# Performance work log

Measured on AMD Instinct MI355X. Metric: run time of the kernel, lower is better.

The kernel has to match this reference:

```python
import jax, jax.numpy as jnp
import numpy as np

B, D, H1, H2 = 512, 1024, 512, 128

def setup_inputs() -> dict:
    key = jax.random.key(0)
    ks = jax.random.split(key, 3)
    x = jax.random.normal(ks[0], (B, D), dtype=jnp.float32)
    W1 = jax.random.normal(ks[1], (H1, D), dtype=jnp.float32)
    W2 = jax.random.normal(ks[2], (H2, H1), dtype=jnp.float32)
    b1 = jnp.full((H1,), 0.1, dtype=jnp.float32)
    b2 = jnp.full((H2,), 0.1, dtype=jnp.float32)
    b3 = jnp.full((H1,), 0.1, dtype=jnp.float32)
    b_r = jnp.full((D,), 0.1, dtype=jnp.float32)
    return {"x": x, "W1": W1, "b1": b1, "W2": W2, "b2": b2, "b3": b3, "b_r": b_r}

def reference(x, W1, b1, W2, b2, b3, b_r):
    # encoder
    c1 = jax.nn.sigmoid(x @ W1.T + b1)          # [B, H1]
    c2 = jax.nn.sigmoid(c1 @ W2.T + b2)         # [B, H2]
    # decoder (tied weights)
    c3 = jax.nn.sigmoid(c2 @ W2 + b3)           # [B, H1]
    recover = c3 @ W1 + b_r                     # [B, D]
    # Jacobian of code w.r.t. x, batched (replaces per-sample diag+matmul loop):
    # Jac[b] = diag(c2'(b)) @ W2 @ diag(c1'(b)) @ W1
    s1p = c1 * (1.0 - c1)                       # [B, H1]
    s2p = c2 * (1.0 - c2)                       # [B, H2]
    M = s2p[:, :, None] * W2[None, :, :] * s1p[:, None, :]   # [B, H2, H1]
    Jac = jnp.einsum('bhk,kd->bhd', M, W1)      # [B, H2, D]
    return (recover, c2, Jac)
```

## Files before the change

kernel.cpp:

```cpp
#include <hip/hip_runtime.h>


typedef _Float16 f16x8 __attribute__((ext_vector_type(8)));
typedef _Float16 f16x4 __attribute__((ext_vector_type(4)));
typedef float    f32x4 __attribute__((ext_vector_type(4)));
typedef float    f32x2 __attribute__((ext_vector_type(2)));

__device__ __forceinline__ void gld_lds16(const _Float16* src, _Float16* dst_wave_uniform) {
    __builtin_amdgcn_global_load_lds((const __attribute__((address_space(1))) unsigned int*)src,
                                     (__attribute__((address_space(3))) unsigned int*)dst_wave_uniform,
                                     16, 0, 0);
}

__device__ __forceinline__ void prep_dev(int bx, const float* __restrict__ W1,
                                         const float* __restrict__ W2,
                                         _Float16* __restrict__ W1T,
                                         _Float16* __restrict__ W2h) {
    if (bx < 512) {
        __shared__ float tile[32][33];
        int dt = (bx & 31) * 32, kt = (bx >> 5) * 32;
        int tx = threadIdx.x & 31, ty = threadIdx.x >> 5;
        #pragma unroll
        for (int r = 0; r < 32; r += 8)
            tile[ty + r][tx] = W1[(kt + ty + r) * 1024 + dt + tx];
        __syncthreads();
        #pragma unroll
        for (int r = 0; r < 32; r += 8)
            W1T[(size_t)(dt + ty + r) * 512 + kt + tx] = (_Float16)tile[tx][ty + r];
    } else {
        int i = (bx - 512) * 1024 + threadIdx.x * 4;
        f32x4 v = *(const f32x4*)(W2 + i);
        f16x4 h;
        h.x = (_Float16)v.x; h.y = (_Float16)v.y; h.z = (_Float16)v.z; h.w = (_Float16)v.w;
        *(f16x4*)(W2h + i) = h;
    }
}

template <int EPI, bool TRANSB>
__device__ void gemm_dev(const float* __restrict__ A, const float* __restrict__ Bm,
                         const float* __restrict__ bias,
                         float* __restrict__ C, float* __restrict__ Cd,
                         _Float16* __restrict__ Ch,
                         int M, int N, int K, int m0, int n0) {
    __shared__ __align__(16) float As[32][34];
    __shared__ __align__(16) float Bs[32][68];
    const int tid = threadIdx.x, tx = tid & 15, ty = tid >> 4;
    const int ka  = tid & 31, ma  = tid >> 5;
    const int kbt = tid & 31, nbt = tid >> 5;
    const int nbf = tid & 63, kbf = tid >> 6;
    float acc[2][4] = {};
    float rA[4], rB[8];

    #pragma unroll
    for (int r = 0; r < 4; ++r) rA[r] = A[(size_t)(m0 + ma + 8 * r) * K + ka];
    if (TRANSB) {
        #pragma unroll
        for (int r = 0; r < 8; ++r) rB[r] = Bm[(size_t)(n0 + nbt + 8 * r) * K + kbt];
    } else {
        #pragma unroll
        for (int r = 0; r < 8; ++r) rB[r] = Bm[(size_t)(kbf + 4 * r) * N + n0 + nbf];
    }

    for (int k0 = 0; k0 < K; k0 += 32) {
        #pragma unroll
        for (int r = 0; r < 4; ++r) As[ka][ma + 8 * r] = rA[r];
        if (TRANSB) {
            #pragma unroll
            for (int r = 0; r < 8; ++r) Bs[kbt][nbt + 8 * r] = rB[r];
        } else {
            #pragma unroll
            for (int r = 0; r < 8; ++r) Bs[kbf + 4 * r][nbf] = rB[r];
        }
        const int k1 = k0 + 32;
        if (k1 < K) {
            #pragma unroll
            for (int r = 0; r < 4; ++r) rA[r] = A[(size_t)(m0 + ma + 8 * r) * K + k1 + ka];
            if (TRANSB) {
                #pragma unroll
                for (int r = 0; r < 8; ++r) rB[r] = Bm[(size_t)(n0 + nbt + 8 * r) * K + k1 + kbt];
            } else {
                #pragma unroll
                for (int r = 0; r < 8; ++r) rB[r] = Bm[(size_t)(k1 + kbf + 4 * r) * N + n0 + nbf];
            }
        }
        __syncthreads();
        #pragma unroll
        for (int k = 0; k < 32; ++k) {
            f32x2 av = *(const f32x2*)&As[k][ty * 2];
            f32x4 bv = *(const f32x4*)&Bs[k][tx * 4];
            #pragma unroll
            for (int i = 0; i < 2; ++i)
                #pragma unroll
                for (int j = 0; j < 4; ++j)
                    acc[i][j] += av[i] * bv[j];
        }
        __syncthreads();
    }

    #pragma unroll
    for (int i = 0; i < 2; ++i) {
        int row = m0 + ty * 2 + i;
        #pragma unroll
        for (int j = 0; j < 4; ++j) {
            int col = n0 + tx * 4 + j;
            float z = acc[i][j] + bias[col];
            float s = 1.f / (1.f + __expf(-z));
            if constexpr (EPI == 1) {
                C[(size_t)row * N + col]  = s;
                Cd[(size_t)row * N + col] = s * (1.f - s);
            } else {
                Ch[(size_t)row * N + col] = (_Float16)s;
            }
        }
    }
}

__global__ __launch_bounds__(256) void fused_prep_gemm1(const float* __restrict__ x,
                                                        const float* __restrict__ W1,
                                                        const float* __restrict__ b1,
                                                        const float* __restrict__ W2,
                                                        _Float16* __restrict__ W1T,
                                                        _Float16* __restrict__ W2h,
                                                        float* __restrict__ c1,
                                                        float* __restrict__ s1p) {
    int bx = blockIdx.x;
    if (bx < 128) {
        gemm_dev<1, true>(x, W1, b1, c1, s1p, nullptr, 512, 512, 1024,
                          (bx >> 3) * 32, (bx & 7) * 64);
    } else {
        prep_dev(bx - 128, W1, W2, W1T, W2h);
    }
}

__global__ __launch_bounds__(256) void gemm2_kernel(const float* __restrict__ c1,
                                                    const float* __restrict__ W2,
                                                    const float* __restrict__ b2,
                                                    float* __restrict__ out_c2,
                                                    float* __restrict__ s2p) {
    gemm_dev<1, true>(c1, W2, b2, out_c2, s2p, nullptr, 512, 128, 512,
                      blockIdx.y * 32, blockIdx.x * 64);
}

__global__ __launch_bounds__(256) void gemm3_kernel(const float* __restrict__ out_c2,
                                                    const float* __restrict__ W2,
                                                    const float* __restrict__ b3,
                                                    _Float16* __restrict__ c3h) {
    gemm_dev<2, false>(out_c2, W2, b3, nullptr, nullptr, c3h, 512, 512, 128,
                       (blockIdx.x >> 3) * 32, (blockIdx.x & 7) * 64);
}

__global__ __launch_bounds__(256, 2) void jacW_fused(const _Float16* __restrict__ c3h,
                                                     const _Float16* __restrict__ W2h,
                                                     const _Float16* __restrict__ W1T,
                                                     const float* __restrict__ s1p,
                                                     const float* __restrict__ s2p,
                                                     const float* __restrict__ br,
                                                     float* __restrict__ out_rec,
                                                     float* __restrict__ out_jac) {
    __shared__ __align__(16) _Float16 Wsl[128 * 64];
    __shared__ __align__(16) _Float16 Bsl[128 * 64];
    __shared__ __align__(16) float    Esl[64][132];
    __shared__ _Float16 S1h[2][512];
    __shared__ float    S2s[2][128];

    const int tid = threadIdx.x;
    const int lane = tid & 63, wave = tid >> 6;
    const int wm = (wave >> 1) * 64, wn = (wave & 1) * 64;
    const int l15 = lane & 15, q = lane >> 4;
    const int bid = blockIdx.x;

    const int srow = wave * 8 + (lane >> 3);
    const int skof = ((lane & 7) ^ (lane >> 3)) * 8;

    if (bid < 32) {
        const int m0 = (bid >> 3) * 128, n0 = (bid & 7) * 128;
        const _Float16* Abase = c3h + (size_t)m0 * 512;
        const _Float16* Bbase = W1T + (size_t)n0 * 512;
        float* outp = out_rec + (size_t)m0 * 1024;
        if (tid < 128) S2s[0][tid] = br[n0 + tid];

        f32x4 acc[4][4];
        #pragma unroll
        for (int i = 0; i < 4; ++i)
            #pragma unroll
            for (int j = 0; j < 4; ++j) acc[i][j] = (f32x4){0.f, 0.f, 0.f, 0.f};

        for (int t = 0; t < 8; ++t) {
            const int kb = t * 64;
            #pragma unroll
            for (int r = 0; r < 4; ++r) {
                gld_lds16(Abase + (size_t)(r * 32 + srow) * 512 + kb + skof, Wsl + (r * 32 + wave * 8) * 64);
                gld_lds16(Bbase + (size_t)(r * 32 + srow) * 512 + kb + skof, Bsl + (r * 32 + wave * 8) * 64);
            }
            __syncthreads();
            #pragma unroll
            for (int kk = 0; kk < 64; kk += 32) {
                f16x8 af[4], bf[4];
                #pragma unroll
                for (int i = 0; i < 4; ++i)
                    af[i] = *(const f16x8*)(Wsl + (wm + i * 16 + l15) * 64 + ((kk + q * 8) ^ ((l15 & 7) * 8)));
                #pragma unroll
                for (int j = 0; j < 4; ++j)
                    bf[j] = *(const f16x8*)(Bsl + (wn + j * 16 + l15) * 64 + ((kk + q * 8) ^ ((l15 & 7) * 8)));
                #pragma unroll
                for (int i = 0; i < 4; ++i)
                    #pragma unroll
                    for (int j = 0; j < 4; ++j)
                        acc[i][j] = __builtin_amdgcn_mfma_f32_16x16x32_f16(af[i], bf[j], acc[i][j], 0, 0, 0);
            }
            __syncthreads();
        }

        #pragma unroll
        for (int i = 0; i < 4; ++i) {
            #pragma unroll
            for (int rg = 0; rg < 4; ++rg) {
                int ml = wm + i * 16 + q * 4 + rg;
                #pragma unroll
                for (int j = 0; j < 4; ++j) {
                    int cl = wn + j * 16 + l15;
                    __builtin_nontemporal_store(acc[i][j][rg] + S2s[0][cl],
                                                outp + (size_t)ml * 1024 + n0 + cl);
                }
            }
        }
        return;
    }

    const int jid = bid - 32;
    const int w = (jid & 7) * 256 + (jid >> 3);
    const int pair = w >> 3, n0 = (w & 7) * 128;
    const int bA = pair * 2;

    S1h[0][tid]       = (_Float16)s1p[(size_t)bA * 512 + tid];
    S1h[0][tid + 256] = (_Float16)s1p[(size_t)bA * 512 + 256 + tid];
    S1h[1][tid]       = (_Float16)s1p[(size_t)(bA + 1) * 512 + tid];
    S1h[1][tid + 256] = (_Float16)s1p[(size_t)(bA + 1) * 512 + 256 + tid];
    if (tid < 128) S2s[0][tid] = s2p[(size_t)bA * 128 + tid];
    else           S2s[1][tid - 128] = s2p[(size_t)(bA + 1) * 128 + (tid - 128)];

    const _Float16* Bbase = W1T + (size_t)n0 * 512;

    f32x4 accA[4][4], accB[4][4];
    #pragma unroll
    for (int i = 0; i < 4; ++i)
        #pragma unroll
        for (int j = 0; j < 4; ++j) {
            accA[i][j] = (f32x4){0.f, 0.f, 0.f, 0.f};
            accB[i][j] = (f32x4){0.f, 0.f, 0.f, 0.f};
        }

    for (int t = 0; t < 8; ++t) {
        const int kb = t * 64;
        #pragma unroll
        for (int r = 0; r < 4; ++r) {
            gld_lds16(W2h   + (size_t)(r * 32 + srow) * 512 + kb + skof, Wsl + (r * 32 + wave * 8) * 64);
            gld_lds16(Bbase + (size_t)(r * 32 + srow) * 512 + kb + skof, Bsl + (r * 32 + wave * 8) * 64);
        }
        __syncthreads();
        #pragma unroll
        for (int kk = 0; kk < 64; kk += 32) {
            const f16x8 sfA = *(const f16x8*)(&S1h[0][kb + kk + q * 8]);
            const f16x8 sfB = *(const f16x8*)(&S1h[1][kb + kk + q * 8]);
            f16x8 bf[4];
            #pragma unroll
            for (int j = 0; j < 4; ++j)
                bf[j] = *(const f16x8*)(Bsl + (wn + j * 16 + l15) * 64 + ((kk + q * 8) ^ ((l15 & 7) * 8)));
            #pragma unroll
            for (int i = 0; i < 4; ++i) {
                const f16x8 wf = *(const f16x8*)(Wsl + (wm + i * 16 + l15) * 64 + ((kk + q * 8) ^ ((l15 & 7) * 8)));
                f16x8 af = wf * sfA;
                #pragma unroll
                for (int j = 0; j < 4; ++j)
                    accA[i][j] = __builtin_amdgcn_mfma_f32_16x16x32_f16(af, bf[j], accA[i][j], 0, 0, 0);
                af = wf * sfB;
                #pragma unroll
                for (int j = 0; j < 4; ++j)
                    accB[i][j] = __builtin_amdgcn_mfma_f32_16x16x32_f16(af, bf[j], accB[i][j], 0, 0, 0);
            }
        }
        __syncthreads();
    }

    float* outA = out_jac + (size_t)bA * (128 * 1024);
    float* outB = outA + (128 * 1024);
    #pragma unroll
    for (int bsel = 0; bsel < 2; ++bsel) {
        float* op = bsel ? outB : outA;
        #pragma unroll
        for (int half = 0; half < 2; ++half) {
            __syncthreads();
            if ((wave >> 1) == half) {
                #pragma unroll
                for (int i = 0; i < 4; ++i) {
                    #pragma unroll
                    for (int rg = 0; rg < 4; ++rg) {
                        const int lr = i * 16 + q * 4 + rg;
                        const float rs = bsel ? S2s[1][half * 64 + lr]
                                              : S2s[0][half * 64 + lr];
                        #pragma unroll
                        for (int j = 0; j < 4; ++j) {
                            const int cl = wn + j * 16 + l15;
                            Esl[lr][cl] = (bsel ? accB[i][j][rg] : accA[i][j][rg]) * rs;
                        }
                    }
                }
            }
            __syncthreads();
            #pragma unroll
            for (int p = 0; p < 8; ++p) {
                const int lr = p * 8 + (tid >> 5);
                const f32x4 v4 = *(const f32x4*)&Esl[lr][(tid & 31) * 4];
                __builtin_nontemporal_store(v4,
                    (f32x4*)(op + (size_t)(half * 64 + lr) * 1024 + n0 + (tid & 31) * 4));
            }
        }
    }
}

extern "C" void kernel_launch(void* const* d_in, const int* in_sizes, int n_in,
                              void* d_out, int out_size, void* d_ws, size_t ws_size,
                              hipStream_t stream) {
    const float* x  = (const float*)d_in[0];
    const float* W1 = (const float*)d_in[1];
    const float* b1 = (const float*)d_in[2];
    const float* W2 = (const float*)d_in[3];
    const float* b2 = (const float*)d_in[4];
    const float* b3 = (const float*)d_in[5];
    const float* br = (const float*)d_in[6];

    float* out_rec = (float*)d_out;
    float* out_c2  = out_rec + 512 * 1024;
    float* out_jac = out_c2 + 512 * 128;

    char* ws = (char*)d_ws;
    _Float16* W1T = (_Float16*)(ws);
    _Float16* W2h = (_Float16*)(ws + 0x100000);
    float*    c1  = (float*)(ws + 0x120000);
    float*    s1p = (float*)(ws + 0x220000);
    float*    s2p = (float*)(ws + 0x320000);
    _Float16* c3h = (_Float16*)(ws + 0x360000);

    fused_prep_gemm1<<<704, 256, 0, stream>>>(x, W1, b1, W2, W1T, W2h, c1, s1p);
    gemm2_kernel<<<dim3(2, 16), 256, 0, stream>>>(c1, W2, b2, out_c2, s2p);
    gemm3_kernel<<<128, 256, 0, stream>>>(out_c2, W2, b3, c3h);
    jacW_fused<<<2080, 256, 0, stream>>>(c3h, W2h, W1T, s1p, s2p, br, out_rec, out_jac);
}
```

Before: 397.2 us.

## Fuse encoder second layer and decoder first layer into one kernel

Replaces the separate gemm2 and gemm3 launches with a single mid_fused kernel that loads 8 rows of c1 into shared memory, computes c2 and s2p, keeps c2 in shared memory, and immediately computes c3 in fp16. This removes one kernel launch and the global round trip of c2 between the two small GEMMs. The trade-off is only 64 blocks with a simple per-thread dot-product scheme that re-reads W2 from global/L2 in every block, so parallelism and compute efficiency drop compared with the tiled GEMM.

Measured after the change: 371.4 us. 6.5% less time.

```diff
diff --git a/kernel.cpp b/kernel.cpp
--- a/kernel.cpp
+++ b/kernel.cpp
@@ -36,52 +36,35 @@
     }
 }
 
-template <int EPI, bool TRANSB>
-__device__ void gemm_dev(const float* __restrict__ A, const float* __restrict__ Bm,
-                         const float* __restrict__ bias,
-                         float* __restrict__ C, float* __restrict__ Cd,
-                         _Float16* __restrict__ Ch,
-                         int M, int N, int K, int m0, int n0) {
+__device__ void gemm_c1(const float* __restrict__ A, const float* __restrict__ Bm,
+                        const float* __restrict__ bias,
+                        float* __restrict__ C, float* __restrict__ Cd,
+                        int m0, int n0) {
+    const int N = 512, K = 1024;
     __shared__ __align__(16) float As[32][34];
     __shared__ __align__(16) float Bs[32][68];
     const int tid = threadIdx.x, tx = tid & 15, ty = tid >> 4;
     const int ka  = tid & 31, ma  = tid >> 5;
     const int kbt = tid & 31, nbt = tid >> 5;
-    const int nbf = tid & 63, kbf = tid >> 6;
     float acc[2][4] = {};
     float rA[4], rB[8];
 
     #pragma unroll
     for (int r = 0; r < 4; ++r) rA[r] = A[(size_t)(m0 + ma + 8 * r) * K + ka];
-    if (TRANSB) {
-        #pragma unroll
-        for (int r = 0; r < 8; ++r) rB[r] = Bm[(size_t)(n0 + nbt + 8 * r) * K + kbt];
-    } else {
-        #pragma unroll
-        for (int r = 0; r < 8; ++r) rB[r] = Bm[(size_t)(kbf + 4 * r) * N + n0 + nbf];
-    }
+    #pragma unroll
+    for (int r = 0; r < 8; ++r) rB[r] = Bm[(size_t)(n0 + nbt + 8 * r) * K + kbt];
 
     for (int k0 = 0; k0 < K; k0 += 32) {
         #pragma unroll
         for (int r = 0; r < 4; ++r) As[ka][ma + 8 * r] = rA[r];
-        if (TRANSB) {
-            #pragma unroll
-            for (int r = 0; r < 8; ++r) Bs[kbt][nbt + 8 * r] = rB[r];
-        } else {
-            #pragma unroll
-            for (int r = 0; r < 8; ++r) Bs[kbf + 4 * r][nbf] = rB[r];
-        }
+        #pragma unroll
+        for (int r = 0; r < 8; ++r) Bs[kbt][nbt + 8 * r] = rB[r];
         const int k1 = k0 + 32;
         if (k1 < K) {
             #pragma unroll
             for (int r = 0; r < 4; ++r) rA[r] = A[(size_t)(m0 + ma + 8 * r) * K + k1 + ka];
-            if (TRANSB) {
-                #pragma unroll
-                for (int r = 0; r < 8; ++r) rB[r] = Bm[(size_t)(n0 + nbt + 8 * r) * K + k1 + kbt];
-            } else {
-                #pragma unroll
-                for (int r = 0; r < 8; ++r) rB[r] = Bm[(size_t)(k1 + kbf + 4 * r) * N + n0 + nbf];
-            }
+            #pragma unroll
+            for (int r = 0; r < 8; ++r) rB[r] = Bm[(size_t)(n0 + nbt + 8 * r) * K + k1 + kbt];
         }
         __syncthreads();
         #pragma unroll
@@ -105,12 +88,8 @@
             int col = n0 + tx * 4 + j;
             float z = acc[i][j] + bias[col];
             float s = 1.f / (1.f + __expf(-z));
-            if constexpr (EPI == 1) {
-                C[(size_t)row * N + col]  = s;
-                Cd[(size_t)row * N + col] = s * (1.f - s);
-            } else {
-                Ch[(size_t)row * N + col] = (_Float16)s;
-            }
+            C[(size_t)row * N + col]  = s;
+            Cd[(size_t)row * N + col] = s * (1.f - s);
         }
     }
 }
@@ -125,28 +104,76 @@
                                                         float* __restrict__ s1p) {
     int bx = blockIdx.x;
     if (bx < 128) {
-        gemm_dev<1, true>(x, W1, b1, c1, s1p, nullptr, 512, 512, 1024,
-                          (bx >> 3) * 32, (bx & 7) * 64);
+        gemm_c1(x, W1, b1, c1, s1p, (bx >> 3) * 32, (bx & 7) * 64);
     } else {
         prep_dev(bx - 128, W1, W2, W1T, W2h);
     }
 }
 
-__global__ __launch_bounds__(256) void gemm2_kernel(const float* __restrict__ c1,
-                                                    const float* __restrict__ W2,
-                                                    const float* __restrict__ b2,
-                                                    float* __restrict__ out_c2,
-                                                    float* __restrict__ s2p) {
-    gemm_dev<1, true>(c1, W2, b2, out_c2, s2p, nullptr, 512, 128, 512,
-                      blockIdx.y * 32, blockIdx.x * 64);
-}
-
-__global__ __launch_bounds__(256) void gemm3_kernel(const float* __restrict__ out_c2,
-                                                    const float* __restrict__ W2,
-                                                    const float* __restrict__ b3,
-                                                    _Float16* __restrict__ c3h) {
-    gemm_dev<2, false>(out_c2, W2, b3, nullptr, nullptr, c3h, 512, 512, 128,
-                       (blockIdx.x >> 3) * 32, (blockIdx.x & 7) * 64);
+__global__ __launch_bounds__(256) void mid_fused(const float* __restrict__ c1,
+                                                 const float* __restrict__ W2,
+                                                 const float* __restrict__ b2,
+                                                 const float* __restrict__ b3,
+                                                 float* __restrict__ out_c2,
+                                                 float* __restrict__ s2p,
+                                                 _Float16* __restrict__ c3h) {
+    __shared__ __align__(16) float C1L[8][512];
+    __shared__ float C2L[8][128];
+    const int tid = threadIdx.x;
+    const int m0 = blockIdx.x * 8;
+
+    {
+        const f32x4* src = (const f32x4*)(c1 + (size_t)m0 * 512);
+        f32x4* dst = (f32x4*)&C1L[0][0];
+        #pragma unroll
+        for (int u = 0; u < 4; ++u) dst[tid + u * 256] = src[tid + u * 256];
+    }
+    __syncthreads();
+
+    {
+        const int h = tid & 127, rg = tid >> 7;
+        const float* w2r = W2 + (size_t)h * 512;
+        float acc[4] = {0.f, 0.f, 0.f, 0.f};
+        for (int k = 0; k < 512; k += 4) {
+            const f32x4 wv = *(const f32x4*)(w2r + k);
+            #pragma unroll
+            for (int r = 0; r < 4; ++r) {
+                const f32x4 cv = *(const f32x4*)&C1L[rg * 4 + r][k];
+                acc[r] += cv.x * wv.x + cv.y * wv.y + cv.z * wv.z + cv.w * wv.w;
+            }
+        }
+        const float bb = b2[h];
+        #pragma unroll
+        for (int r = 0; r < 4; ++r) {
+            const int row = rg * 4 + r;
+            const float s = 1.f / (1.f + __expf(-(acc[r] + bb)));
+            out_c2[(size_t)(m0 + row) * 128 + h] = s;
+            s2p[(size_t)(m0 + row) * 128 + h]    = s * (1.f - s);
+            C2L[row][h] = s;
+        }
+    }
+    __syncthreads();
+
+    {
+        const int j0 = tid, j1 = tid + 256;
+        float a0[8] = {}, a1[8] = {};
+        for (int h = 0; h < 128; ++h) {
+            const float w0 = W2[(size_t)h * 512 + j0];
+            const float w1 = W2[(size_t)h * 512 + j1];
+            #pragma unroll
+            for (int r = 0; r < 8; ++r) {
+                const float c = C2L[r][h];
+                a0[r] += c * w0;
+                a1[r] += c * w1;
+            }
+        }
+        const float bb0 = b3[j0], bb1 = b3[j1];
+        #pragma unroll
+        for (int r = 0; r < 8; ++r) {
+            c3h[(size_t)(m0 + r) * 512 + j0] = (_Float16)(1.f / (1.f + __expf(-(a0[r] + bb0))));
+            c3h[(size_t)(m0 + r) * 512 + j1] = (_Float16)(1.f / (1.f + __expf(-(a1[r] + bb1))));
+        }
+    }
 }
 
 __global__ __launch_bounds__(256, 2) void jacW_fused(const _Float16* __restrict__ c3h,
@@ -342,7 +369,6 @@
     _Float16* c3h = (_Float16*)(ws + 0x360000);
 
     fused_prep_gemm1<<<704, 256, 0, stream>>>(x, W1, b1, W2, W1T, W2h, c1, s1p);
-    gemm2_kernel<<<dim3(2, 16), 256, 0, stream>>>(c1, W2, b2, out_c2, s2p);
-    gemm3_kernel<<<128, 256, 0, stream>>>(out_c2, W2, b3, c3h);
+    mid_fused<<<64, 256, 0, stream>>>(c1, W2, b2, b3, out_c2, s2p, c3h);
     jacW_fused<<<2080, 256, 0, stream>>>(c3h, W2h, W1T, s1p, s2p, br, out_rec, out_jac);
 }
```
